# Kernel tuning notes

Measured on AMD Instinct MI355X. Metric: run time of the kernel, lower is better.

## Reference

```python
import jax, jax.numpy as jnp
import numpy as np

C_IN = 1024
C_INTER = 512
EPS = 1e-5
STD = 0.01


def _conv1x1(x, w, b):
    # x: [B,C,H,W], w: [O,C] (1x1 conv kernel squeezed), b: [O]
    return jnp.einsum('bchw,oc->bohw', x, w) + b[None, :, None, None]


def setup_inputs() -> dict:
    key = jax.random.key(0)
    ks = jax.random.split(key, 12)
    def w(k, o, i):
        return jax.random.normal(k, (o, i), jnp.float32) * STD
    def b(k, o):
        return jax.random.normal(k, (o,), jnp.float32) * STD
    return {
        'x': jax.random.normal(ks[0], (8, C_IN, 64, 64), jnp.float32),
        'theta_w': w(ks[1], C_INTER, C_IN), 'theta_b': b(ks[2], C_INTER),
        'phi_w': w(ks[3], C_INTER, C_IN), 'phi_b': b(ks[4], C_INTER),
        'g_w': w(ks[5], C_INTER, C_IN), 'g_b': b(ks[6], C_INTER),
        'wz_w': w(ks[7], C_IN, C_INTER), 'wz_b': b(ks[8], C_IN),
        'bn_gamma': jax.random.normal(ks[9], (C_IN,), jnp.float32) * 0.1,
        'bn_beta': jax.random.normal(ks[10], (C_IN,), jnp.float32) * 0.1,
    }


def reference(x, theta_w, theta_b, phi_w, phi_b, g_w, g_b, wz_w, wz_b, bn_gamma, bn_beta):
    B, C, H, W = x.shape
    # theta on full-res input: [B, Ci, H*W]
    theta = _conv1x1(x, theta_w, theta_b).reshape(B, C_INTER, H * W)
    # 2x2 stride-2 max pool for phi/g path
    xp = jax.lax.reduce_window(x, -jnp.inf, jax.lax.max,
                               (1, 1, 2, 2), (1, 1, 2, 2), 'VALID')
    Hp, Wp = xp.shape[2], xp.shape[3]
    phi = _conv1x1(xp, phi_w, phi_b).reshape(B, C_INTER, Hp * Wp)
    g = _conv1x1(xp, g_w, g_b).reshape(B, C_INTER, Hp * Wp)
    # attention: [B, H*W, Hp*Wp], scaled softmax
    attn = jnp.einsum('bcn,bcm->bnm', theta, phi) * (C_INTER ** -0.5)
    attn = jax.nn.softmax(attn, axis=-1)
    # aggregate: [B, Ci, H*W]
    y = jnp.einsum('bcm,bnm->bcn', g, attn).reshape(B, C_INTER, H, W)
    z = _conv1x1(y, wz_w, wz_b)
    # BatchNorm2d (training-mode batch stats, biased var)
    mean = z.mean(axis=(0, 2, 3), keepdims=True)
    var = jnp.mean((z - mean) ** 2, axis=(0, 2, 3), keepdims=True)
    z = (z - mean) * jax.lax.rsqrt(var + EPS)
    z = z * bn_gamma[None, :, None, None] + bn_beta[None, :, None, None]
    return x + z
```

## Files before the change

kernel.cpp:

```cpp
#include <hip/hip_runtime.h>

typedef unsigned short u16;
typedef unsigned int u32;
typedef __attribute__((ext_vector_type(8))) short bf16x8;
typedef __attribute__((ext_vector_type(4))) float f32x4;

__device__ __forceinline__ u16 f2bf(float f) {
  u32 u = __builtin_bit_cast(u32, f);
  u = u + 0x7FFFu + ((u >> 16) & 1u);
  return (u16)(u >> 16);
}
__device__ __forceinline__ float bf2f(u16 s) {
  return __builtin_bit_cast(float, (u32)s << 16);
}

__device__ __forceinline__ void gload_lds16(const u16* g, u16* l) {
  __builtin_amdgcn_global_load_lds(
      (const __attribute__((address_space(1))) u32*)g,
      (__attribute__((address_space(3))) u32*)l, 16, 0, 0);
}

__global__ __launch_bounds__(256) void k_cvt(const float* __restrict__ s,
                                             u16* __restrict__ d) {
  int i = (blockIdx.x * 256 + threadIdx.x) * 4;
  float4 v = *(const float4*)(s + i);
  u32 lo = (u32)f2bf(v.x) | ((u32)f2bf(v.y) << 16);
  u32 hi = (u32)f2bf(v.z) | ((u32)f2bf(v.w) << 16);
  uint2 o; o.x = lo; o.y = hi;
  *(uint2*)(d + i) = o;
}

__global__ __launch_bounds__(256) void k_transpose_pool(
    const float* __restrict__ x, u16* __restrict__ xT, u16* __restrict__ xpT) {
  __shared__ u16 lds[128 * 64];
  const int t = threadIdx.x;
  const int c0 = blockIdx.x * 64;
  const int by = blockIdx.y;
  const int b = blockIdx.z;

  {
    const int nf = (t & 31) * 4;
    const int swz = 8 * (t & 7);
    const float* xb =
        x + ((size_t)(b * 1024 + c0 + (t >> 5)) * 4096) + by * 128 + nf;
#pragma unroll
    for (int u = 0; u < 8; ++u) {
      const int c_l = (t >> 5) + 8 * u;
      float4 v = *(const float4*)(xb + (size_t)(8 * u) * 4096);
      const int col = c_l ^ swz;
      lds[(nf + 0) * 64 + col] = f2bf(v.x);
      lds[(nf + 1) * 64 + col] = f2bf(v.y);
      lds[(nf + 2) * 64 + col] = f2bf(v.z);
      lds[(nf + 3) * 64 + col] = f2bf(v.w);
    }
  }
  __syncthreads();
  {
#pragma unroll
    for (int v = 0; v < 4; ++v) {
      const int idx = t + 256 * v;
      const int n_l = idx >> 3;
      const int cb = (idx & 7) * 8;
      const int col = cb ^ (8 * ((n_l >> 2) & 7));
      bf16x8 d = *(const bf16x8*)&lds[n_l * 64 + col];
      *(bf16x8*)&xT[((size_t)b * 4096 + by * 128 + n_l) * 1024 + c0 + cb] = d;
    }
  }
  {
    const int m_w = t >> 3;
    const int cb = (t & 7) * 8;
    const int na = 2 * m_w, nb = na + 1, nc = na + 64, nd = na + 65;
    bf16x8 va = *(const bf16x8*)&lds[na * 64 + (cb ^ (8 * ((na >> 2) & 7)))];
    bf16x8 vb = *(const bf16x8*)&lds[nb * 64 + (cb ^ (8 * ((nb >> 2) & 7)))];
    bf16x8 vc = *(const bf16x8*)&lds[nc * 64 + (cb ^ (8 * ((nc >> 2) & 7)))];
    bf16x8 vd = *(const bf16x8*)&lds[nd * 64 + (cb ^ (8 * ((nd >> 2) & 7)))];
    bf16x8 o;
#pragma unroll
    for (int j = 0; j < 8; ++j) {
      float m = fmaxf(fmaxf(bf2f((u16)va[j]), bf2f((u16)vb[j])),
                      fmaxf(bf2f((u16)vc[j]), bf2f((u16)vd[j])));
      o[j] = (short)f2bf(m);
    }
    *(bf16x8*)&xpT[((size_t)b * 1024 + by * 32 + m_w) * 1024 + c0 + cb] = o;
  }
}

template <int BIAS_MODE>
__global__ __launch_bounds__(512) void gemm256(
    const u16* __restrict__ A, long aBS, const u16* __restrict__ Bm, long bBS,
    u16* __restrict__ Cm, long cBS, const float* __restrict__ bias, int N,
    int K, float scale) {
  __shared__ u16 ALDS[2][16384];
  __shared__ u16 BLDS[2][16384];
  const int t = threadIdx.x;
  u32 gx = gridDim.x, gy = gridDim.y;
  u32 nwg = gx * gy * gridDim.z;
  u32 wg = blockIdx.x + gx * (blockIdx.y + gy * blockIdx.z);
  u32 swz = (wg & 7) * (nwg >> 3) + (wg >> 3);
  const int bn = swz % gx;
  u32 tmp = swz / gx;
  const int bm = tmp % gy;
  const int b = tmp / gy;

  const u16* Agb = A + (size_t)b * aBS + (size_t)bm * 256 * K;
  const u16* Bgb = Bm + (size_t)b * bBS + (size_t)bn * 256 * K;

  const int lane = t & 63;
  const int wid = t >> 6;
  const int wr = wid >> 2;
  const int wc = wid & 3;
  const int lr = lane & 15;
  const int kg = (lane >> 4) & 3;
  const int T = K >> 6;

  f32x4 acc[8][4] = {};

#define STAGE_G(LDSARR, GB, h, ktn)                                          \
  if ((ktn) < T) {                                                           \
    {                                                                        \
      const int r = t >> 3;                                                  \
      gload_lds16(GB + (size_t)((h)*128 + r) * K + (size_t)(ktn)*64 +        \
                      (((t & 7) ^ (r & 7)) * 8),                             \
                  &LDSARR[(ktn) & 1][(h)*8192 + t * 8]);                     \
    }                                                                        \
    {                                                                        \
      const int idx = 512 + t;                                               \
      const int r = idx >> 3;                                                \
      gload_lds16(GB + (size_t)((h)*128 + r) * K + (size_t)(ktn)*64 +        \
                      (((t & 7) ^ (r & 7)) * 8),                             \
                  &LDSARR[(ktn) & 1][(h)*8192 + idx * 8]);                   \
    }                                                                        \
  }
#define STAGE_A(h, ktn) STAGE_G(ALDS, Agb, h, ktn)
#define STAGE_B(h, ktn) STAGE_G(BLDS, Bgb, h, ktn)

#define LDA4(mh, kk)                                                         \
  _Pragma("unroll") for (int m2 = 0; m2 < 4; ++m2) {                         \
    const int row = wr * 128 + ((mh)*4 + m2) * 16 + lr;                      \
    aF[m2] = *(const bf16x8*)&ALDS[cb][row * 64 +                            \
                                       ((((kk)*4 + kg) ^ (lr & 7)) * 8)];    \
  }
#define LDB4(kk)                                                             \
  _Pragma("unroll") for (int n = 0; n < 4; ++n) {                            \
    const int row = wc * 64 + n * 16 + lr;                                   \
    bF[n] = *(const bf16x8*)&BLDS[cb][row * 64 +                             \
                                      ((((kk)*4 + kg) ^ (lr & 7)) * 8)];     \
  }
#define MFMA16(M0)                                                           \
  __builtin_amdgcn_s_setprio(1);                                             \
  _Pragma("unroll") for (int n = 0; n < 4; ++n) {                            \
    acc[(M0) + 0][n] = __builtin_amdgcn_mfma_f32_16x16x32_bf16(              \
        aF[0], bF[n], acc[(M0) + 0][n], 0, 0, 0);                            \
    acc[(M0) + 1][n] = __builtin_amdgcn_mfma_f32_16x16x32_bf16(              \
        aF[1], bF[n], acc[(M0) + 1][n], 0, 0, 0);                            \
    acc[(M0) + 2][n] = __builtin_amdgcn_mfma_f32_16x16x32_bf16(              \
        aF[2], bF[n], acc[(M0) + 2][n], 0, 0, 0);                            \
    acc[(M0) + 3][n] = __builtin_amdgcn_mfma_f32_16x16x32_bf16(              \
        aF[3], bF[n], acc[(M0) + 3][n], 0, 0, 0);                            \
  }                                                                          \
  __builtin_amdgcn_s_setprio(0);
#define CFENCE asm volatile("" ::: "memory")

  STAGE_B(0, 0);
  STAGE_B(1, 0);
  STAGE_A(0, 0);
  STAGE_A(1, 0);
  STAGE_B(0, 1);

  for (int kt = 0; kt < T; ++kt) {
    const int cb = kt & 1;
    bf16x8 aF[4], bF[4];
    asm volatile("s_waitcnt vmcnt(2)" ::: "memory");
    __builtin_amdgcn_s_barrier();
    STAGE_B(1, kt + 1);
    LDB4(0);
    LDA4(0, 0);
    MFMA16(0);
    CFENCE;
    __builtin_amdgcn_s_barrier();
    STAGE_A(0, kt + 1);
    LDA4(1, 0);
    MFMA16(4);
    CFENCE;
    __builtin_amdgcn_s_barrier();
    STAGE_A(1, kt + 1);
    LDB4(1);
    LDA4(0, 1);
    MFMA16(0);
    CFENCE;
    __builtin_amdgcn_s_barrier();
    STAGE_B(0, kt + 2);
    LDA4(1, 1);
    MFMA16(4);
    CFENCE;
    __builtin_amdgcn_s_barrier();
  }

  u16* Cb = Cm + (size_t)b * cBS;
#pragma unroll
  for (int m = 0; m < 8; ++m) {
    const int row0 = bm * 256 + wr * 128 + m * 16 + kg * 4;
#pragma unroll
    for (int n = 0; n < 4; ++n) {
      const int col = bn * 256 + wc * 64 + n * 16 + lr;
      float bj = (BIAS_MODE == 2) ? bias[col] : 0.f;
#pragma unroll
      for (int r = 0; r < 4; ++r) {
        float v = acc[m][n][r] * scale;
        if (BIAS_MODE == 1) v += bias[row0 + r];
        if (BIAS_MODE == 2) v += bj;
        Cb[(size_t)(row0 + r) * N + col] = f2bf(v);
      }
    }
  }
#undef STAGE_G
#undef STAGE_A
#undef STAGE_B
#undef LDA4
#undef LDB4
#undef MFMA16
#undef CFENCE
}

__global__ __launch_bounds__(256) void k_softmax(u16* __restrict__ S) {
  const int t = threadIdx.x;
  const int lane = t & 63;
  const size_t row = (size_t)blockIdx.x * 4 + (t >> 6);
  u16* p = S + row * 1024 + lane * 16;
  uint4 d0 = *(const uint4*)p;
  uint4 d1 = *(const uint4*)(p + 8);
  u32 u[8] = {d0.x, d0.y, d0.z, d0.w, d1.x, d1.y, d1.z, d1.w};
  float v[16];
#pragma unroll
  for (int i = 0; i < 8; ++i) {
    v[2 * i] = bf2f((u16)(u[i] & 0xffff));
    v[2 * i + 1] = bf2f((u16)(u[i] >> 16));
  }
  float m = v[0];
#pragma unroll
  for (int i = 1; i < 16; ++i) m = fmaxf(m, v[i]);
  for (int o = 32; o > 0; o >>= 1) m = fmaxf(m, __shfl_xor(m, o));
  const float LOG2E = 1.44269504088896f;
  float s = 0.f;
#pragma unroll
  for (int i = 0; i < 16; ++i) {
    v[i] = exp2f((v[i] - m) * LOG2E);
    s += v[i];
  }
  for (int o = 32; o > 0; o >>= 1) s += __shfl_xor(s, o);
  float inv = 1.0f / s;
#pragma unroll
  for (int i = 0; i < 8; ++i)
    u[i] = (u32)f2bf(v[2 * i] * inv) | ((u32)f2bf(v[2 * i + 1] * inv) << 16);
  uint4 o0; o0.x = u[0]; o0.y = u[1]; o0.z = u[2]; o0.w = u[3];
  uint4 o1; o1.x = u[4]; o1.y = u[5]; o1.z = u[6]; o1.w = u[7];
  *(uint4*)p = o0;
  *(uint4*)(p + 8) = o1;
}

__global__ __launch_bounds__(256) void k_stats(const u16* __restrict__ z,
                                               float2* __restrict__ stats) {
  const int o = blockIdx.x;
  const int t = threadIdx.x;
  float s = 0.f, q = 0.f;
  for (int b = 0; b < 8; ++b) {
    const u16* p = z + ((size_t)b * 1024 + o) * 4096;
    for (int i = t * 4; i < 4096; i += 1024) {
      uint2 d = *(const uint2*)(p + i);
      float a0 = bf2f((u16)(d.x & 0xffff)), a1 = bf2f((u16)(d.x >> 16));
      float a2 = bf2f((u16)(d.y & 0xffff)), a3 = bf2f((u16)(d.y >> 16));
      s += a0 + a1 + a2 + a3;
      q += a0 * a0 + a1 * a1 + a2 * a2 + a3 * a3;
    }
  }
  for (int o2 = 32; o2 > 0; o2 >>= 1) {
    s += __shfl_xor(s, o2);
    q += __shfl_xor(q, o2);
  }
  __shared__ float2 red[4];
  if ((t & 63) == 0) red[t >> 6] = make_float2(s, q);
  __syncthreads();
  if (t == 0) {
    float S_ = 0.f, Q_ = 0.f;
    for (int i = 0; i < 4; ++i) { S_ += red[i].x; Q_ += red[i].y; }
    stats[o] = make_float2(S_, Q_);
  }
}

__global__ __launch_bounds__(256) void k_apply(
    const float* __restrict__ x, const u16* __restrict__ z,
    const float2* __restrict__ stats, const float* __restrict__ gamma,
    const float* __restrict__ beta, float* __restrict__ out) {
  size_t i4 = (size_t)blockIdx.x * 256 + threadIdx.x;
  size_t e = i4 * 4;
  int c = (int)((e >> 12) & 1023);
  float2 st = stats[c];
  const float cnt = 1.0f / 32768.0f;
  float mean = st.x * cnt;
  float var = st.y * cnt - mean * mean;
  float g = rsqrtf(var + 1e-5f) * gamma[c];
  float sh = beta[c] - mean * g;
  float4 xv = *(const float4*)(x + e);
  uint2 zd = *(const uint2*)(z + e);
  float z0 = bf2f((u16)(zd.x & 0xffff)), z1 = bf2f((u16)(zd.x >> 16));
  float z2 = bf2f((u16)(zd.y & 0xffff)), z3 = bf2f((u16)(zd.y >> 16));
  float4 ov;
  ov.x = xv.x + z0 * g + sh;
  ov.y = xv.y + z1 * g + sh;
  ov.z = xv.z + z2 * g + sh;
  ov.w = xv.w + z3 * g + sh;
  *(float4*)(out + e) = ov;
}

extern "C" void kernel_launch(void* const* d_in, const int* in_sizes, int n_in,
                              void* d_out, int out_size, void* d_ws,
                              size_t ws_size, hipStream_t stream) {
  const float* x = (const float*)d_in[0];
  const float* theta_w = (const float*)d_in[1];
  const float* theta_b = (const float*)d_in[2];
  const float* phi_w = (const float*)d_in[3];
  const float* phi_b = (const float*)d_in[4];
  const float* g_w = (const float*)d_in[5];
  const float* g_b = (const float*)d_in[6];
  const float* wz_w = (const float*)d_in[7];
  const float* wz_b = (const float*)d_in[8];
  const float* gamma = (const float*)d_in[9];
  const float* beta = (const float*)d_in[10];
  float* out = (float*)d_out;

  char* w = (char*)d_ws;
  const size_t MiB = (size_t)1 << 20;
  u16* WT = (u16*)(w + 0 * MiB);
  u16* WP = (u16*)(w + 1 * MiB);
  u16* WG = (u16*)(w + 2 * MiB);
  u16* WZ = (u16*)(w + 3 * MiB);
  u16* XT = (u16*)(w + 4 * MiB);
  u16* XPT = (u16*)(w + 68 * MiB);
  u16* THETA = (u16*)(w + 84 * MiB);
  u16* PHI = (u16*)(w + 116 * MiB);
  u16* G = (u16*)(w + 124 * MiB);
  u16* S = XT;
  u16* YT = (u16*)(w + 132 * MiB);
  u16* Z = S;
  float2* stats = (float2*)(w + 164 * MiB);

  k_cvt<<<512, 256, 0, stream>>>(theta_w, WT);
  k_cvt<<<512, 256, 0, stream>>>(phi_w, WP);
  k_cvt<<<512, 256, 0, stream>>>(g_w, WG);
  k_cvt<<<512, 256, 0, stream>>>(wz_w, WZ);
  k_transpose_pool<<<dim3(16, 32, 8), 256, 0, stream>>>(x, XT, XPT);
  gemm256<2><<<dim3(2, 128, 1), 512, 0, stream>>>(
      XT, 0, WT, 0, THETA, 0, theta_b, 512, 1024, 1.0f);
  gemm256<2><<<dim3(2, 32, 1), 512, 0, stream>>>(
      XPT, 0, WP, 0, PHI, 0, phi_b, 512, 1024, 1.0f);
  gemm256<1><<<dim3(4, 2, 8), 512, 0, stream>>>(
      WG, 0, XPT, (long)1024 * 1024, G, (long)512 * 1024, g_b, 1024, 1024,
      1.0f);
  gemm256<0><<<dim3(4, 16, 8), 512, 0, stream>>>(
      THETA, (long)4096 * 512, PHI, (long)1024 * 512, S, (long)4096 * 1024,
      nullptr, 1024, 512, 0.04419417382415922f);
  k_softmax<<<8192, 256, 0, stream>>>(S);
  gemm256<0><<<dim3(2, 16, 8), 512, 0, stream>>>(
      S, (long)4096 * 1024, G, (long)512 * 1024, YT, (long)4096 * 512, nullptr,
      512, 1024, 1.0f);
  gemm256<1><<<dim3(16, 4, 8), 512, 0, stream>>>(
      WZ, 0, YT, (long)4096 * 512, Z, (long)1024 * 4096, wz_b, 4096, 512,
      1.0f);
  k_stats<<<1024, 256, 0, stream>>>(Z, stats);
  k_apply<<<32768, 256, 0, stream>>>(x, Z, stats, gamma, beta, out);

  (void)in_sizes; (void)n_in; (void)out_size; (void)ws_size;
}
```

Measured before the change: 631.6 us.

## Fuse BN statistics into final GEMM epilogue and retile phi/g projections

Batch-norm sums and squared sums are accumulated with shuffle reductions and atomics in the epilogue of the output-projection GEMM, which removes the separate stats pass over Z. A new 128x128-tile GEMM replaces the 256x256 kernel for the pooled phi and g projections so those grids launch more blocks. The four weight conversions are merged into one launch, and a zeroing kernel is added for the atomic accumulators. Stats are now taken from fp32 values before rounding, and the atomics add some contention.

```diff
diff --git a/kernel.cpp b/kernel.cpp
--- a/kernel.cpp
+++ b/kernel.cpp
@@ -20,14 +20,26 @@
       (__attribute__((address_space(3))) u32*)l, 16, 0, 0);
 }
 
-__global__ __launch_bounds__(256) void k_cvt(const float* __restrict__ s,
-                                             u16* __restrict__ d) {
-  int i = (blockIdx.x * 256 + threadIdx.x) * 4;
-  float4 v = *(const float4*)(s + i);
+__global__ __launch_bounds__(512) void k_zero(float* __restrict__ p) {
+  float4 z = {0.f, 0.f, 0.f, 0.f};
+  *(float4*)(p + threadIdx.x * 4) = z;
+}
+
+__global__ __launch_bounds__(256) void k_cvt4(
+    const float* __restrict__ s0, const float* __restrict__ s1,
+    const float* __restrict__ s2, const float* __restrict__ s3,
+    u16* __restrict__ d0, u16* __restrict__ d1, u16* __restrict__ d2,
+    u16* __restrict__ d3) {
+  int gid = blockIdx.x * 256 + threadIdx.x;
+  int which = gid >> 17;
+  int loc = (gid & 131071) * 4;
+  const float* s = which == 0 ? s0 : which == 1 ? s1 : which == 2 ? s2 : s3;
+  u16* d = which == 0 ? d0 : which == 1 ? d1 : which == 2 ? d2 : d3;
+  float4 v = *(const float4*)(s + loc);
   u32 lo = (u32)f2bf(v.x) | ((u32)f2bf(v.y) << 16);
   u32 hi = (u32)f2bf(v.z) | ((u32)f2bf(v.w) << 16);
   uint2 o; o.x = lo; o.y = hi;
-  *(uint2*)(d + i) = o;
+  *(uint2*)(d + loc) = o;
 }
 
 __global__ __launch_bounds__(256) void k_transpose_pool(
@@ -86,10 +98,88 @@
 }
 
 template <int BIAS_MODE>
+__global__ __launch_bounds__(256, 2) void gemm_nt(
+    const u16* __restrict__ A, long aBS, const u16* __restrict__ Bm, long bBS,
+    u16* __restrict__ Cm, long cBS, const float* __restrict__ bias, int N,
+    int K, float scale) {
+  __shared__ u16 Alds[2][128 * 32];
+  __shared__ u16 Blds[2][128 * 32];
+  const int t = threadIdx.x;
+  const int b = blockIdx.z;
+  const int bm = blockIdx.y, bn = blockIdx.x;
+  const u16* Ab = A + (size_t)b * aBS + (size_t)bm * 128 * K;
+  const u16* Bb = Bm + (size_t)b * bBS + (size_t)bn * 128 * K;
+
+  const int lane = t & 63;
+  const int w = t >> 6;
+  const int wrow = w >> 1, wcol = w & 1;
+  const int lr = lane & 15;
+  const int kg = lane >> 4;
+
+  f32x4 acc[4][4] = {};
+
+  const int e0 = t * 8;
+  const int r0 = e0 >> 5;
+  const int k0i = e0 & 31;
+  const int steps = K >> 5;
+
+#define STAGE(buf, ks)                                                   \
+  do {                                                                   \
+    const int kb = (ks) * 32;                                            \
+    gload_lds16(Ab + (size_t)r0 * K + kb + k0i, &Alds[buf][e0]);         \
+    gload_lds16(Ab + (size_t)(r0 + 64) * K + kb + k0i,                   \
+                &Alds[buf][e0 + 2048]);                                  \
+    gload_lds16(Bb + (size_t)r0 * K + kb + k0i, &Blds[buf][e0]);         \
+    gload_lds16(Bb + (size_t)(r0 + 64) * K + kb + k0i,                   \
+                &Blds[buf][e0 + 2048]);                                  \
+  } while (0)
+
+  STAGE(0, 0);
+  for (int ks = 0; ks < steps; ++ks) {
+    const int cur = ks & 1;
+    __syncthreads();
+    if (ks + 1 < steps) STAGE(cur ^ 1, ks + 1);
+    bf16x8 af[4], bfr[4];
+#pragma unroll
+    for (int i = 0; i < 4; ++i) {
+      af[i] =
+          *(const bf16x8*)&Alds[cur][(wrow * 64 + i * 16 + lr) * 32 + kg * 8];
+      bfr[i] =
+          *(const bf16x8*)&Blds[cur][(wcol * 64 + i * 16 + lr) * 32 + kg * 8];
+    }
+#pragma unroll
+    for (int i = 0; i < 4; ++i)
+#pragma unroll
+      for (int j = 0; j < 4; ++j)
+        acc[i][j] = __builtin_amdgcn_mfma_f32_16x16x32_bf16(af[i], bfr[j],
+                                                            acc[i][j], 0, 0, 0);
+  }
+#undef STAGE
+
+  u16* Cb = Cm + (size_t)b * cBS;
+#pragma unroll
+  for (int i = 0; i < 4; ++i) {
+#pragma unroll
+    for (int j = 0; j < 4; ++j) {
+      int row0 = bm * 128 + wrow * 64 + i * 16 + kg * 4;
+      int col = bn * 128 + wcol * 64 + j * 16 + lr;
+      float bj = (BIAS_MODE == 2) ? bias[col] : 0.f;
+#pragma unroll
+      for (int r = 0; r < 4; ++r) {
+        float v = acc[i][j][r] * scale;
+        if (BIAS_MODE == 1) v += bias[row0 + r];
+        if (BIAS_MODE == 2) v += bj;
+        Cb[(size_t)(row0 + r) * N + col] = f2bf(v);
+      }
+    }
+  }
+}
+
+template <int BIAS_MODE, int STATS>
 __global__ __launch_bounds__(512) void gemm256(
     const u16* __restrict__ A, long aBS, const u16* __restrict__ Bm, long bBS,
     u16* __restrict__ Cm, long cBS, const float* __restrict__ bias, int N,
-    int K, float scale) {
+    int K, float scale, float* __restrict__ statsp) {
   __shared__ u16 ALDS[2][16384];
   __shared__ u16 BLDS[2][16384];
   const int t = threadIdx.x;
@@ -197,19 +287,50 @@
   }
 
   u16* Cb = Cm + (size_t)b * cBS;
-#pragma unroll
-  for (int m = 0; m < 8; ++m) {
-    const int row0 = bm * 256 + wr * 128 + m * 16 + kg * 4;
-#pragma unroll
-    for (int n = 0; n < 4; ++n) {
-      const int col = bn * 256 + wc * 64 + n * 16 + lr;
-      float bj = (BIAS_MODE == 2) ? bias[col] : 0.f;
+  if constexpr (!STATS) {
+#pragma unroll
+    for (int m = 0; m < 8; ++m) {
+      const int row0 = bm * 256 + wr * 128 + m * 16 + kg * 4;
+#pragma unroll
+      for (int n = 0; n < 4; ++n) {
+        const int col = bn * 256 + wc * 64 + n * 16 + lr;
+        float bj = (BIAS_MODE == 2) ? bias[col] : 0.f;
+#pragma unroll
+        for (int r = 0; r < 4; ++r) {
+          float v = acc[m][n][r] * scale;
+          if (BIAS_MODE == 1) v += bias[row0 + r];
+          if (BIAS_MODE == 2) v += bj;
+          Cb[(size_t)(row0 + r) * N + col] = f2bf(v);
+        }
+      }
+    }
+  } else {
+#pragma unroll
+    for (int m = 0; m < 8; ++m) {
+      const int row0 = bm * 256 + wr * 128 + m * 16 + kg * 4;
 #pragma unroll
       for (int r = 0; r < 4; ++r) {
-        float v = acc[m][n][r] * scale;
-        if (BIAS_MODE == 1) v += bias[row0 + r];
-        if (BIAS_MODE == 2) v += bj;
-        Cb[(size_t)(row0 + r) * N + col] = f2bf(v);
+        const int row = row0 + r;
+        float bi = (BIAS_MODE == 1) ? bias[row] : 0.f;
+        float s = 0.f, q = 0.f;
+#pragma unroll
+        for (int n = 0; n < 4; ++n) {
+          const int col = bn * 256 + wc * 64 + n * 16 + lr;
+          float v = acc[m][n][r] * scale + bi;
+          if (BIAS_MODE == 2) v += bias[col];
+          Cb[(size_t)row * N + col] = f2bf(v);
+          s += v;
+          q += v * v;
+        }
+#pragma unroll
+        for (int off = 1; off < 16; off <<= 1) {
+          s += __shfl_xor(s, off);
+          q += __shfl_xor(q, off);
+        }
+        if (lr == 0) {
+          atomicAdd(&statsp[2 * row], s);
+          atomicAdd(&statsp[2 * row + 1], q);
+        }
       }
     }
   }
@@ -256,35 +377,6 @@
   uint4 o1; o1.x = u[4]; o1.y = u[5]; o1.z = u[6]; o1.w = u[7];
   *(uint4*)p = o0;
   *(uint4*)(p + 8) = o1;
-}
-
-__global__ __launch_bounds__(256) void k_stats(const u16* __restrict__ z,
-                                               float2* __restrict__ stats) {
-  const int o = blockIdx.x;
-  const int t = threadIdx.x;
-  float s = 0.f, q = 0.f;
-  for (int b = 0; b < 8; ++b) {
-    const u16* p = z + ((size_t)b * 1024 + o) * 4096;
-    for (int i = t * 4; i < 4096; i += 1024) {
-      uint2 d = *(const uint2*)(p + i);
-      float a0 = bf2f((u16)(d.x & 0xffff)), a1 = bf2f((u16)(d.x >> 16));
-      float a2 = bf2f((u16)(d.y & 0xffff)), a3 = bf2f((u16)(d.y >> 16));
-      s += a0 + a1 + a2 + a3;
-      q += a0 * a0 + a1 * a1 + a2 * a2 + a3 * a3;
-    }
-  }
-  for (int o2 = 32; o2 > 0; o2 >>= 1) {
-    s += __shfl_xor(s, o2);
-    q += __shfl_xor(q, o2);
-  }
-  __shared__ float2 red[4];
-  if ((t & 63) == 0) red[t >> 6] = make_float2(s, q);
-  __syncthreads();
-  if (t == 0) {
-    float S_ = 0.f, Q_ = 0.f;
-    for (int i = 0; i < 4; ++i) { S_ += red[i].x; Q_ += red[i].y; }
-    stats[o] = make_float2(S_, Q_);
-  }
 }
 
 __global__ __launch_bounds__(256) void k_apply(
@@ -342,32 +434,31 @@
   u16* S = XT;
   u16* YT = (u16*)(w + 132 * MiB);
   u16* Z = S;
-  float2* stats = (float2*)(w + 164 * MiB);
-
-  k_cvt<<<512, 256, 0, stream>>>(theta_w, WT);
-  k_cvt<<<512, 256, 0, stream>>>(phi_w, WP);
-  k_cvt<<<512, 256, 0, stream>>>(g_w, WG);
-  k_cvt<<<512, 256, 0, stream>>>(wz_w, WZ);
+  float* stats = (float*)(w + 164 * MiB);
+
+  k_zero<<<1, 512, 0, stream>>>(stats);
+  k_cvt4<<<2048, 256, 0, stream>>>(theta_w, phi_w, g_w, wz_w, WT, WP, WG, WZ);
   k_transpose_pool<<<dim3(16, 32, 8), 256, 0, stream>>>(x, XT, XPT);
-  gemm256<2><<<dim3(2, 128, 1), 512, 0, stream>>>(
-      XT, 0, WT, 0, THETA, 0, theta_b, 512, 1024, 1.0f);
-  gemm256<2><<<dim3(2, 32, 1), 512, 0, stream>>>(
-      XPT, 0, WP, 0, PHI, 0, phi_b, 512, 1024, 1.0f);
-  gemm256<1><<<dim3(4, 2, 8), 512, 0, stream>>>(
+  gemm256<2, 0><<<dim3(2, 128, 1), 512, 0, stream>>>(
+      XT, 0, WT, 0, THETA, 0, theta_b, 512, 1024, 1.0f, nullptr);
+  gemm_nt<2><<<dim3(4, 8, 8), 256, 0, stream>>>(
+      XPT, (long)1024 * 1024, WP, 0, PHI, (long)1024 * 512, phi_b, 512, 1024,
+      1.0f);
+  gemm_nt<1><<<dim3(8, 4, 8), 256, 0, stream>>>(
       WG, 0, XPT, (long)1024 * 1024, G, (long)512 * 1024, g_b, 1024, 1024,
       1.0f);
-  gemm256<0><<<dim3(4, 16, 8), 512, 0, stream>>>(
+  gemm256<0, 0><<<dim3(4, 16, 8), 512, 0, stream>>>(
       THETA, (long)4096 * 512, PHI, (long)1024 * 512, S, (long)4096 * 1024,
-      nullptr, 1024, 512, 0.04419417382415922f);
+      nullptr, 1024, 512, 0.04419417382415922f, nullptr);
   k_softmax<<<8192, 256, 0, stream>>>(S);
-  gemm256<0><<<dim3(2, 16, 8), 512, 0, stream>>>(
+  gemm256<0, 0><<<dim3(2, 16, 8), 512, 0, stream>>>(
       S, (long)4096 * 1024, G, (long)512 * 1024, YT, (long)4096 * 512, nullptr,
-      512, 1024, 1.0f);
-  gemm256<1><<<dim3(16, 4, 8), 512, 0, stream>>>(
-      WZ, 0, YT, (long)4096 * 512, Z, (long)1024 * 4096, wz_b, 4096, 512,
-      1.0f);
-  k_stats<<<1024, 256, 0, stream>>>(Z, stats);
-  k_apply<<<32768, 256, 0, stream>>>(x, Z, stats, gamma, beta, out);
+      512, 1024, 1.0f, nullptr);
+  gemm256<1, 1><<<dim3(16, 4, 8), 512, 0, stream>>>(
+      WZ, 0, YT, (long)4096 * 512, Z, (long)1024 * 4096, wz_b, 4096, 512, 1.0f,
+      stats);
+  k_apply<<<32768, 256, 0, stream>>>(x, Z, (const float2*)stats, gamma, beta,
+                                     out);
 
   (void)in_sizes; (void)n_in; (void)out_size; (void)ws_size;
 }
```

After: 801.7 us. 1.27x slower.
